# Kernel tuning notes

Hardware: AMD Instinct MI355X
Metric: run time of the kernel (lower is better)

## Reference

```python
import jax, jax.numpy as jnp
import numpy as np

B = 2048
C = 32            # num_categories
STATE_DIM = 64    # state_input_dim
EMB = 256         # emb_dim
OUT = 256         # output_dim
OBS_DIM = 512


def _cat_linear(x, W_all, b_all, cat_ids):
    # x: [B,S,din]; W_all: [C,din,dout]; b_all: [C,dout]; cat_ids: [B]
    W = W_all[cat_ids]            # [B,din,dout]  (per-sample weight gather)
    b = b_all[cat_ids]            # [B,dout]
    return jnp.einsum('bsd,bdh->bsh', x, W) + b[:, None, :]


def setup_inputs() -> dict:
    key = jax.random.key(0)
    ks = jax.random.split(key, 8)
    state = jax.random.normal(ks[0], (B, STATE_DIM), dtype=jnp.float32)
    obs = jax.random.uniform(ks[1], (B, 1, OBS_DIM), dtype=jnp.float32)
    cat_ids = jax.random.randint(ks[2], (B,), 0, C)
    obs_W = 0.01 * jax.random.normal(ks[3], (OBS_DIM, EMB), dtype=jnp.float32)
    obs_b = jnp.zeros((EMB,), dtype=jnp.float32)
    state_W = 0.02 * jax.random.normal(ks[4], (C, STATE_DIM, EMB), dtype=jnp.float32)
    state_b = jnp.zeros((C, EMB), dtype=jnp.float32)
    l2_W = 0.02 * jax.random.normal(ks[5], (C, 2 * EMB, OUT), dtype=jnp.float32)
    l2_b = jnp.zeros((C, OUT), dtype=jnp.float32)
    return {"state": state, "obs": obs, "cat_ids": cat_ids,
            "obs_W": obs_W, "obs_b": obs_b,
            "state_W": state_W, "state_b": state_b,
            "l2_W": l2_W, "l2_b": l2_b}


def reference(state, obs, cat_ids, obs_W, obs_b, state_W, state_b, l2_W, l2_b):
    # ObsEncoder (modeled as a linear projection): [B,1,OBS_DIM] -> [B,1,EMB]
    obs_emb = jnp.einsum('bsd,dh->bsh', obs, obs_W) + obs_b
    # state: [B,STATE_DIM] -> [B,1,STATE_DIM]
    state3 = state[:, None, :]
    state_emb = jax.nn.relu(_cat_linear(state3, state_W, state_b, cat_ids))  # [B,1,EMB]
    x = jnp.concatenate((state_emb, obs_emb), axis=2)                        # [B,1,2*EMB]
    return _cat_linear(x, l2_W, l2_b, cat_ids)                               # [B,1,OUT]
```

## Files before the change

kernel.cpp:

```cpp
#include <hip/hip_runtime.h>

constexpr int B_N   = 2048;
constexpr int C_N   = 32;
constexpr int SD    = 64;
constexpr int EMB   = 256;
constexpr int OUTD  = 256;
constexpr int OBSD  = 512;
constexpr int XDIM  = 512;
constexpr int CAP   = 256;

typedef __attribute__((ext_vector_type(8))) short bf16x8;
typedef __attribute__((ext_vector_type(4))) short bf16x4;
typedef __attribute__((ext_vector_type(4))) float f32x4;

constexpr size_t OFF_ROWS  = 4096;
constexpr size_t OFF_POBS  = 65536;
constexpr size_t OFF_PSTAT = 327680;
constexpr size_t OFF_PL2   = 1376256;
constexpr size_t NEED_L2   = OFF_PL2 + (size_t)C_N * XDIM * OUTD * 2;

__device__ __forceinline__ unsigned short bf_cvt(float f) {
    union { float f; unsigned u; } x; x.f = f;
    unsigned r = x.u + 0x7FFF + ((x.u >> 16) & 1);
    return (unsigned short)(r >> 16);
}

__global__ __launch_bounds__(256) void prep_kernel(
    const int* __restrict__ cat_ids,
    const float* __restrict__ obs_W, const float* __restrict__ state_W,
    const float* __restrict__ l2_W,
    int* __restrict__ counts, int* __restrict__ rows,
    unsigned short* __restrict__ p_obs, unsigned short* __restrict__ p_state,
    unsigned short* __restrict__ p_l2, int do_l2) {
    const int bid = blockIdx.x;
    const int t = threadIdx.x;

    if (bid < C_N) {
        __shared__ int cnt;
        __shared__ int list[CAP];
        if (t == 0) cnt = 0;
        __syncthreads();
        const int c = bid;
        for (int r = t; r < B_N; r += 256) {
            if (cat_ids[r] == c) {
                int s = atomicAdd(&cnt, 1);
                if (s < CAP) list[s] = r;
            }
        }
        __syncthreads();
        int n = min(cnt, CAP);
        for (int s = t; s < n; s += 256) rows[c * CAP + s] = list[s];
        if (t == 0) counts[c] = n;
        return;
    }

    const float* src;
    unsigned short* dst;
    {
        int pb = bid - C_N;
        if (pb < 16) {
            src = obs_W + (size_t)pb * 32 * 256;
            dst = p_obs + (size_t)pb * 8192;
        } else if (pb < 80) {
            int i = pb - 16;
            int mat = i >> 1, ch = i & 1;
            src = state_W + ((size_t)mat * SD + ch * 32) * 256;
            dst = p_state + (size_t)i * 8192;
        } else {
            if (!do_l2) return;
            int i = pb - 80;
            int mat = i >> 4, ch = i & 15;
            src = l2_W + ((size_t)mat * XDIM + ch * 32) * 256;
            dst = p_l2 + (size_t)i * 8192;
        }
    }

    __shared__ __align__(16) unsigned short sW[32 * 264];
    #pragma unroll
    for (int i2 = 0; i2 < 8; ++i2) {
        int f = t + 256 * i2;
        int row = f >> 6, c4 = f & 63;
        float4 v = ((const float4*)src)[f];
        unsigned short* d = &sW[row * 264 + c4 * 4];
        d[0] = bf_cvt(v.x); d[1] = bf_cvt(v.y); d[2] = bf_cvt(v.z); d[3] = bf_cvt(v.w);
    }
    __syncthreads();
    #pragma unroll
    for (int s4 = 0; s4 < 4; ++s4) {
        int slot = s4 * 256 + t;
        int strip = slot >> 6, lane = slot & 63;
        int r0 = (lane >> 4) * 8, col = strip * 16 + (lane & 15);
        unsigned short v[8];
        #pragma unroll
        for (int j = 0; j < 8; ++j) v[j] = sW[(r0 + j) * 264 + col];
        *(bf16x8*)(dst + (size_t)slot * 8) = *(bf16x8*)v;
    }
}

__global__ __launch_bounds__(256) void fused_kernel(
    const float* __restrict__ state, const float* __restrict__ obs,
    const float* __restrict__ obs_b, const float* __restrict__ state_b,
    const float* __restrict__ l2_W, const float* __restrict__ l2_b,
    const int* __restrict__ counts, const int* __restrict__ rows,
    const unsigned short* __restrict__ p_obs,
    const unsigned short* __restrict__ p_state,
    const unsigned short* __restrict__ p_l2, int has_pl2,
    float* __restrict__ out) {
    const int c = blockIdx.x;
    const int tile = blockIdx.y;
    const int n = counts[c];
    const int rbase = tile * 8;
    if (rbase >= n) return;
    const int nr = min(8, n - rbase);

    __shared__ __align__(16) unsigned short sAs[16 * 72];
    __shared__ __align__(16) unsigned short sAo[16 * 520];
    __shared__ __align__(16) unsigned short sX[16 * 520];
    __shared__ int sRows[16];

    const int t = threadIdx.x;
    if (t < 16) sRows[t] = (t < nr) ? rows[c * CAP + rbase + t] : 0;
    __syncthreads();

    {
        int i = t >> 4, c4 = t & 15;
        unsigned short vv[4] = {0, 0, 0, 0};
        if (i < nr) {
            float4 v = ((const float4*)(state + (size_t)sRows[i] * SD))[c4];
            vv[0] = bf_cvt(v.x); vv[1] = bf_cvt(v.y); vv[2] = bf_cvt(v.z); vv[3] = bf_cvt(v.w);
        }
        *(bf16x4*)&sAs[i * 72 + c4 * 4] = *(bf16x4*)vv;
    }
    #pragma unroll
    for (int i2 = 0; i2 < 8; ++i2) {
        int f = t + 256 * i2;
        int i = f >> 7, c4 = f & 127;
        unsigned short vv[4] = {0, 0, 0, 0};
        if (i < nr) {
            float4 v = ((const float4*)(obs + (size_t)sRows[i] * OBSD))[c4];
            vv[0] = bf_cvt(v.x); vv[1] = bf_cvt(v.y); vv[2] = bf_cvt(v.z); vv[3] = bf_cvt(v.w);
        }
        *(bf16x4*)&sAo[i * 520 + c4 * 4] = *(bf16x4*)vv;
    }
    __syncthreads();

    const int w = t >> 6, l = t & 63;
    const int ml = l & 15, quad = l >> 4;

    {
        f32x4 acc[4];
        #pragma unroll
        for (int si = 0; si < 4; ++si) acc[si] = (f32x4){0.f, 0.f, 0.f, 0.f};
        const bf16x8* pb = (const bf16x8*)(p_state + (size_t)c * SD * 256);
        #pragma unroll
        for (int kk = 0; kk < 2; ++kk) {
            bf16x8 a = *(const bf16x8*)&sAs[ml * 72 + kk * 32 + quad * 8];
            #pragma unroll
            for (int si = 0; si < 4; ++si) {
                int strip = w * 4 + si;
                bf16x8 b = pb[(kk * 16 + strip) * 64 + l];
                acc[si] = __builtin_amdgcn_mfma_f32_16x16x32_bf16(a, b, acc[si], 0, 0, 0);
            }
        }
        #pragma unroll
        for (int si = 0; si < 4; ++si) {
            int colb = (w * 4 + si) * 16 + ml;
            float bias = state_b[c * 256 + colb];
            #pragma unroll
            for (int r = 0; r < 4; ++r) {
                int row = quad * 4 + r;
                sX[row * 520 + colb] = bf_cvt(fmaxf(acc[si][r] + bias, 0.f));
            }
        }
    }

    {
        f32x4 acc[4];
        #pragma unroll
        for (int si = 0; si < 4; ++si) acc[si] = (f32x4){0.f, 0.f, 0.f, 0.f};
        const bf16x8* pb = (const bf16x8*)p_obs;
        #pragma unroll
        for (int kk = 0; kk < 16; ++kk) {
            bf16x8 a = *(const bf16x8*)&sAo[ml * 520 + kk * 32 + quad * 8];
            #pragma unroll
            for (int si = 0; si < 4; ++si) {
                int strip = w * 4 + si;
                bf16x8 b = pb[(kk * 16 + strip) * 64 + l];
                acc[si] = __builtin_amdgcn_mfma_f32_16x16x32_bf16(a, b, acc[si], 0, 0, 0);
            }
        }
        #pragma unroll
        for (int si = 0; si < 4; ++si) {
            int colb = (w * 4 + si) * 16 + ml;
            float bias = obs_b[colb];
            #pragma unroll
            for (int r = 0; r < 4; ++r) {
                int row = quad * 4 + r;
                sX[row * 520 + 256 + colb] = bf_cvt(acc[si][r] + bias);
            }
        }
    }
    __syncthreads();

    {
        f32x4 acc[4];
        #pragma unroll
        for (int si = 0; si < 4; ++si) acc[si] = (f32x4){0.f, 0.f, 0.f, 0.f};
        if (has_pl2) {
            const bf16x8* pb = (const bf16x8*)p_l2 + (size_t)c * 16384;
            #pragma unroll
            for (int kk = 0; kk < 16; ++kk) {
                bf16x8 a = *(const bf16x8*)&sX[ml * 520 + kk * 32 + quad * 8];
                #pragma unroll
                for (int si = 0; si < 4; ++si) {
                    int strip = w * 4 + si;
                    bf16x8 b = pb[(kk * 16 + strip) * 64 + l];
                    acc[si] = __builtin_amdgcn_mfma_f32_16x16x32_bf16(a, b, acc[si], 0, 0, 0);
                }
            }
        } else {
            for (int kk = 0; kk < 16; ++kk) {
                bf16x8 a = *(const bf16x8*)&sX[ml * 520 + kk * 32 + quad * 8];
                #pragma unroll
                for (int si = 0; si < 4; ++si) {
                    int strip = w * 4 + si;
                    const float* wsrc = l2_W + ((size_t)c * XDIM + kk * 32 + quad * 8) * 256
                                        + strip * 16 + ml;
                    bf16x8 b;
                    #pragma unroll
                    for (int j = 0; j < 8; ++j) b[j] = (short)bf_cvt(wsrc[j * 256]);
                    acc[si] = __builtin_amdgcn_mfma_f32_16x16x32_bf16(a, b, acc[si], 0, 0, 0);
                }
            }
        }
        #pragma unroll
        for (int si = 0; si < 4; ++si) {
            int colb = (w * 4 + si) * 16 + ml;
            float bias = l2_b[c * 256 + colb];
            #pragma unroll
            for (int r = 0; r < 4; ++r) {
                int row = quad * 4 + r;
                if (row < nr)
                    out[(size_t)sRows[row] * 256 + colb] = acc[si][r] + bias;
            }
        }
    }
}

extern "C" void kernel_launch(void* const* d_in, const int* in_sizes, int n_in,
                              void* d_out, int out_size, void* d_ws, size_t ws_size,
                              hipStream_t stream) {
    const float* state   = (const float*)d_in[0];
    const float* obs     = (const float*)d_in[1];
    const int*   cat_ids = (const int*)d_in[2];
    const float* obs_W   = (const float*)d_in[3];
    const float* obs_b   = (const float*)d_in[4];
    const float* state_W = (const float*)d_in[5];
    const float* state_b = (const float*)d_in[6];
    const float* l2_W    = (const float*)d_in[7];
    const float* l2_b    = (const float*)d_in[8];
    float* out = (float*)d_out;

    char* ws = (char*)d_ws;
    int* counts  = (int*)ws;
    int* rowsbuf = (int*)(ws + OFF_ROWS);
    unsigned short* p_obs  = (unsigned short*)(ws + OFF_POBS);
    unsigned short* p_stat = (unsigned short*)(ws + OFF_PSTAT);
    unsigned short* p_l2   = (unsigned short*)(ws + OFF_PL2);
    const int do_l2 = (ws_size >= NEED_L2) ? 1 : 0;

    int prep_blocks = C_N + 16 + 64 + (do_l2 ? 512 : 0);
    prep_kernel<<<dim3(prep_blocks), dim3(256), 0, stream>>>(
        cat_ids, obs_W, state_W, l2_W, counts, rowsbuf, p_obs, p_stat, p_l2, do_l2);

    fused_kernel<<<dim3(C_N, CAP / 8), dim3(256), 0, stream>>>(
        state, obs, obs_b, state_b, l2_W, l2_b, counts, rowsbuf,
        p_obs, p_stat, p_l2, do_l2, out);
}
```

Before: 120.2 us.

## Double block size to 8 waves and software-prefetch B fragments into registers

Blocks grow from 256 to 512 threads, so each wave covers 2 column strips instead of 4 and per-wave MFMA work is halved. Weight fragments for the state and obs GEMMs are loaded into registers before the input staging barrier. The obs and L2 loops use a 4-deep register ring that prefetches kk+4 while computing kk, hiding global latency behind the row gather and MFMAs. The cost is higher register pressure and more waves per block, each repeating the same A-operand LDS reads.

Result: faster. 99.50 us (-17.2%).

```diff
diff --git a/kernel.cpp b/kernel.cpp
--- a/kernel.cpp
+++ b/kernel.cpp
@@ -97,7 +97,7 @@
     }
 }
 
-__global__ __launch_bounds__(256) void fused_kernel(
+__global__ __launch_bounds__(512) void fused_kernel(
     const float* __restrict__ state, const float* __restrict__ obs,
     const float* __restrict__ obs_b, const float* __restrict__ state_b,
     const float* __restrict__ l2_W, const float* __restrict__ l2_b,
@@ -119,10 +119,30 @@
     __shared__ int sRows[16];
 
     const int t = threadIdx.x;
-    if (t < 16) sRows[t] = (t < nr) ? rows[c * CAP + rbase + t] : 0;
-    __syncthreads();
-
-    {
+    const int w = t >> 6, l = t & 63;
+    const int ml = l & 15, quad = l >> 4;
+
+    if (t < 16) sRows[t] = 0;
+    __syncthreads();
+    if (t < nr) sRows[t] = rows[c * CAP + rbase + t];
+
+    const bf16x8* pb1 = (const bf16x8*)(p_state + (size_t)c * SD * 256);
+    const bf16x8* pb2 = (const bf16x8*)p_obs;
+    bf16x8 pf1[4], pf2[8];
+    #pragma unroll
+    for (int kk = 0; kk < 2; ++kk)
+        #pragma unroll
+        for (int si = 0; si < 2; ++si)
+            pf1[kk * 2 + si] = pb1[(kk * 16 + w * 2 + si) * 64 + l];
+    #pragma unroll
+    for (int kk = 0; kk < 4; ++kk)
+        #pragma unroll
+        for (int si = 0; si < 2; ++si)
+            pf2[kk * 2 + si] = pb2[(kk * 16 + w * 2 + si) * 64 + l];
+
+    __syncthreads();
+
+    if (t < 256) {
         int i = t >> 4, c4 = t & 15;
         unsigned short vv[4] = {0, 0, 0, 0};
         if (i < nr) {
@@ -132,8 +152,8 @@
         *(bf16x4*)&sAs[i * 72 + c4 * 4] = *(bf16x4*)vv;
     }
     #pragma unroll
-    for (int i2 = 0; i2 < 8; ++i2) {
-        int f = t + 256 * i2;
+    for (int i2 = 0; i2 < 4; ++i2) {
+        int f = t + 512 * i2;
         int i = f >> 7, c4 = f & 127;
         unsigned short vv[4] = {0, 0, 0, 0};
         if (i < nr) {
@@ -144,77 +164,76 @@
     }
     __syncthreads();
 
-    const int w = t >> 6, l = t & 63;
-    const int ml = l & 15, quad = l >> 4;
-
-    {
-        f32x4 acc[4];
-        #pragma unroll
-        for (int si = 0; si < 4; ++si) acc[si] = (f32x4){0.f, 0.f, 0.f, 0.f};
-        const bf16x8* pb = (const bf16x8*)(p_state + (size_t)c * SD * 256);
+    {
+        f32x4 acc[2];
+        #pragma unroll
+        for (int si = 0; si < 2; ++si) acc[si] = (f32x4){0.f, 0.f, 0.f, 0.f};
         #pragma unroll
         for (int kk = 0; kk < 2; ++kk) {
             bf16x8 a = *(const bf16x8*)&sAs[ml * 72 + kk * 32 + quad * 8];
             #pragma unroll
-            for (int si = 0; si < 4; ++si) {
-                int strip = w * 4 + si;
-                bf16x8 b = pb[(kk * 16 + strip) * 64 + l];
-                acc[si] = __builtin_amdgcn_mfma_f32_16x16x32_bf16(a, b, acc[si], 0, 0, 0);
-            }
-        }
-        #pragma unroll
-        for (int si = 0; si < 4; ++si) {
-            int colb = (w * 4 + si) * 16 + ml;
+            for (int si = 0; si < 2; ++si)
+                acc[si] = __builtin_amdgcn_mfma_f32_16x16x32_bf16(a, pf1[kk * 2 + si], acc[si], 0, 0, 0);
+        }
+        #pragma unroll
+        for (int si = 0; si < 2; ++si) {
+            int colb = (w * 2 + si) * 16 + ml;
             float bias = state_b[c * 256 + colb];
             #pragma unroll
-            for (int r = 0; r < 4; ++r) {
-                int row = quad * 4 + r;
-                sX[row * 520 + colb] = bf_cvt(fmaxf(acc[si][r] + bias, 0.f));
-            }
-        }
-    }
-
-    {
-        f32x4 acc[4];
-        #pragma unroll
-        for (int si = 0; si < 4; ++si) acc[si] = (f32x4){0.f, 0.f, 0.f, 0.f};
-        const bf16x8* pb = (const bf16x8*)p_obs;
+            for (int r = 0; r < 4; ++r)
+                sX[(quad * 4 + r) * 520 + colb] = bf_cvt(fmaxf(acc[si][r] + bias, 0.f));
+        }
+    }
+
+    {
+        f32x4 acc[2];
+        #pragma unroll
+        for (int si = 0; si < 2; ++si) acc[si] = (f32x4){0.f, 0.f, 0.f, 0.f};
         #pragma unroll
         for (int kk = 0; kk < 16; ++kk) {
             bf16x8 a = *(const bf16x8*)&sAo[ml * 520 + kk * 32 + quad * 8];
             #pragma unroll
-            for (int si = 0; si < 4; ++si) {
-                int strip = w * 4 + si;
-                bf16x8 b = pb[(kk * 16 + strip) * 64 + l];
+            for (int si = 0; si < 2; ++si) {
+                bf16x8 b = pf2[(kk & 3) * 2 + si];
+                if (kk < 12)
+                    pf2[(kk & 3) * 2 + si] = pb2[((kk + 4) * 16 + w * 2 + si) * 64 + l];
                 acc[si] = __builtin_amdgcn_mfma_f32_16x16x32_bf16(a, b, acc[si], 0, 0, 0);
             }
         }
         #pragma unroll
-        for (int si = 0; si < 4; ++si) {
-            int colb = (w * 4 + si) * 16 + ml;
+        for (int si = 0; si < 2; ++si) {
+            int colb = (w * 2 + si) * 16 + ml;
             float bias = obs_b[colb];
             #pragma unroll
-            for (int r = 0; r < 4; ++r) {
-                int row = quad * 4 + r;
-                sX[row * 520 + 256 + colb] = bf_cvt(acc[si][r] + bias);
-            }
-        }
-    }
-    __syncthreads();
-
-    {
-        f32x4 acc[4];
-        #pragma unroll
-        for (int si = 0; si < 4; ++si) acc[si] = (f32x4){0.f, 0.f, 0.f, 0.f};
+            for (int r = 0; r < 4; ++r)
+                sX[(quad * 4 + r) * 520 + 256 + colb] = bf_cvt(acc[si][r] + bias);
+        }
+    }
+
+    const bf16x8* pb3 = (const bf16x8*)p_l2 + (size_t)c * 16384;
+    bf16x8 pf3[8];
+    if (has_pl2) {
+        #pragma unroll
+        for (int kk = 0; kk < 4; ++kk)
+            #pragma unroll
+            for (int si = 0; si < 2; ++si)
+                pf3[kk * 2 + si] = pb3[(kk * 16 + w * 2 + si) * 64 + l];
+    }
+    __syncthreads();
+
+    {
+        f32x4 acc[2];
+        #pragma unroll
+        for (int si = 0; si < 2; ++si) acc[si] = (f32x4){0.f, 0.f, 0.f, 0.f};
         if (has_pl2) {
-            const bf16x8* pb = (const bf16x8*)p_l2 + (size_t)c * 16384;
             #pragma unroll
             for (int kk = 0; kk < 16; ++kk) {
                 bf16x8 a = *(const bf16x8*)&sX[ml * 520 + kk * 32 + quad * 8];
                 #pragma unroll
-                for (int si = 0; si < 4; ++si) {
-                    int strip = w * 4 + si;
-                    bf16x8 b = pb[(kk * 16 + strip) * 64 + l];
+                for (int si = 0; si < 2; ++si) {
+                    bf16x8 b = pf3[(kk & 3) * 2 + si];
+                    if (kk < 12)
+                        pf3[(kk & 3) * 2 + si] = pb3[((kk + 4) * 16 + w * 2 + si) * 64 + l];
                     acc[si] = __builtin_amdgcn_mfma_f32_16x16x32_bf16(a, b, acc[si], 0, 0, 0);
                 }
             }
@@ -222,10 +241,9 @@
             for (int kk = 0; kk < 16; ++kk) {
                 bf16x8 a = *(const bf16x8*)&sX[ml * 520 + kk * 32 + quad * 8];
                 #pragma unroll
-                for (int si = 0; si < 4; ++si) {
-                    int strip = w * 4 + si;
+                for (int si = 0; si < 2; ++si) {
                     const float* wsrc = l2_W + ((size_t)c * XDIM + kk * 32 + quad * 8) * 256
-                                        + strip * 16 + ml;
+                                        + (w * 2 + si) * 16 + ml;
                     bf16x8 b;
                     #pragma unroll
                     for (int j = 0; j < 8; ++j) b[j] = (short)bf_cvt(wsrc[j * 256]);
@@ -234,8 +252,8 @@
             }
         }
         #pragma unroll
-        for (int si = 0; si < 4; ++si) {
-            int colb = (w * 4 + si) * 16 + ml;
+        for (int si = 0; si < 2; ++si) {
+            int colb = (w * 2 + si) * 16 + ml;
             float bias = l2_b[c * 256 + colb];
             #pragma unroll
             for (int r = 0; r < 4; ++r) {
@@ -273,7 +291,7 @@
     prep_kernel<<<dim3(prep_blocks), dim3(256), 0, stream>>>(
         cat_ids, obs_W, state_W, l2_W, counts, rowsbuf, p_obs, p_stat, p_l2, do_l2);
 
-    fused_kernel<<<dim3(C_N, CAP / 8), dim3(256), 0, stream>>>(
+    fused_kernel<<<dim3(C_N, CAP / 8), dim3(512), 0, stream>>>(
         state, obs, obs_b, state_b, l2_W, l2_b, counts, rowsbuf,
         p_obs, p_stat, p_l2, do_l2, out);
 }
```
